# Performance work log

Hardware: AMD Instinct MI355X
Metric: run time of the kernel (lower is better)

The kernel has to match this reference:

```python
import jax, jax.numpy as jnp
import numpy as np

NB_CLS, NB_QRY, NB_SHOT, FEAT_DIM = 5, 75, 5, 640
Q_STEPS, LR_DNI, HID = 3, 1e-3, 4096
N = NB_CLS + NB_QRY           # nodes in similarity graph (80)
M = 1 + N                     # subgraph size (81)
# strict upper triangle of MxM minus the query-query block (matches triu_index_input)
_t = np.ones((M, M)); _t[1 + NB_CLS:, 1 + NB_CLS:] = 0
_t = np.triu(_t, 1)
MASK_IDX = jnp.asarray(np.flatnonzero(_t.ravel() == 1))
DNI_IN = int(MASK_IDX.shape[0])  # 465


def _pairwise(supp, query):
    feat = jnp.concatenate([supp, query], 0)
    nrm = jnp.maximum(jnp.linalg.norm(feat, axis=-1, keepdims=True), 1e-12)
    feat = feat / nrm
    sim = feat @ feat.T                      # (N, N)
    sim_ss = sim[:NB_CLS, :NB_CLS]
    sim_qq = sim[NB_CLS:, NB_CLS:]
    sim_sq = sim[:NB_CLS, NB_CLS:]
    sim_feat_support = jnp.concatenate([sim_ss, sim_sq], 1).T   # (N, nb_cls)
    sim_feat_query = jnp.concatenate([sim_sq, sim_qq], 0)       # (N, nb_qry)
    return sim_feat_support, sim_feat_query, sim_sq


def _subgraph(sim_s, sim_q):
    # topk indices are constants wrt grad (no_grad in torch; ints in jax)
    idx_q = jax.lax.top_k(sim_q, NB_QRY)[1] + NB_CLS
    idx_s = jax.lax.top_k(sim_s, NB_CLS)[1]
    index = jnp.concatenate([jnp.arange(N, dtype=idx_s.dtype)[:, None], idx_s, idx_q], 1)  # (N, M)
    sim = jnp.concatenate([sim_s, sim_q], 1)                     # (N, N)
    sub = sim[index[:, :, None], index[:, None, :]]              # (N, M, M) batched gather
    return sub.reshape(N, M * M)[:, MASK_IDX]                    # (N, DNI_IN)


def _dni(x, W1, b1, W2, b2, W3, b3):
    h = jax.nn.relu(x @ W1.T + b1)
    h = jax.nn.relu(h @ W2.T + b2)
    return h @ W3.T + b3


def _refine(supp, query, ds, dq):
    for _ in range(Q_STEPS):
        inputs, vjp = jax.vjp(lambda s: _subgraph(*_pairwise(s, query)[:2]), supp)
        supp = supp - LR_DNI * vjp(_dni(inputs, *ds))[0]
        inputs, vjp = jax.vjp(lambda q: _subgraph(*_pairwise(supp, q)[:2]), query)
        query = query - LR_DNI * vjp(_dni(inputs, *dq))[0]
    return supp, query


def setup_inputs() -> dict:
    key = jax.random.key(0)
    ks = jax.random.split(key, 16)
    d = {
        "feat_support": jax.random.normal(ks[0], (NB_CLS, NB_SHOT, FEAT_DIM), jnp.float32),
        "feat_query": jax.random.normal(ks[1], (NB_QRY, FEAT_DIM), jnp.float32),
        "scale_cls": jnp.full((1,), 10.0, jnp.float32),
    }
    names = ["ds_W1", "ds_b1", "ds_W2", "ds_b2", "ds_W3", "ds_b3",
             "dq_W1", "dq_b1", "dq_W2", "dq_b2", "dq_W3", "dq_b3"]
    shapes = [(HID, DNI_IN), (HID,), (HID, HID), (HID,), (DNI_IN, HID), (DNI_IN,)] * 2
    for i, (n, sh) in enumerate(zip(names, shapes)):
        d[n] = jax.random.normal(ks[2 + i], sh, jnp.float32) * 0.02
    return d


def reference(feat_support, feat_query, scale_cls,
              ds_W1, ds_b1, ds_W2, ds_b2, ds_W3, ds_b3,
              dq_W1, dq_b1, dq_W2, dq_b2, dq_W3, dq_b3):
    supp = feat_support.mean(1)                                  # (nb_cls, feat_dim)
    ds = (ds_W1, ds_b1, ds_W2, ds_b2, ds_W3, ds_b3)
    dq = (dq_W1, dq_b1, dq_W2, dq_b2, dq_W3, dq_b3)
    supp, query = _refine(supp, feat_query, ds, dq)
    _, _, sim_sq = _pairwise(supp, query)
    return (sim_sq * scale_cls).T                                # (nb_qry, nb_cls)
```

## Files before the change

### kernel.cpp

```cpp
#include <hip/hip_runtime.h>

#define NCLS 5
#define NQRY 75
#define NTOT 80
#define FD   640
#define HIDN 4096
#define DNIN 465
#define KPAD 512
#define NPAD 512
#define LRDNI 1e-3f

#define KS1 4
#define KS2 16
#define KS3 32

typedef short  v8s __attribute__((ext_vector_type(8)));
typedef float  v4f __attribute__((ext_vector_type(4)));

__device__ __forceinline__ ushort f2bf(float x) {
    uint u = __float_as_uint(x);
    u = (u + 0x7FFFu + ((u >> 16) & 1u)) >> 16;
    return (ushort)u;
}
__device__ __forceinline__ uint pk2(float a, float b) {
    return (uint)f2bf(a) | ((uint)f2bf(b) << 16);
}

__global__ void k_setup(const float* __restrict__ fs, const float* __restrict__ fq,
                        const float* __restrict__ W1s, const float* __restrict__ W1q,
                        const float* __restrict__ W2s, const float* __restrict__ W2q,
                        const float* __restrict__ W3s, const float* __restrict__ W3q,
                        ushort* __restrict__ W1bs, ushort* __restrict__ W1bq,
                        ushort* __restrict__ W2bs, ushort* __restrict__ W2bq,
                        ushort* __restrict__ W3bs, ushort* __restrict__ W3bq,
                        float* __restrict__ supp, float* __restrict__ qbuf) {
    int stride = gridDim.x * 256;
    int tid = blockIdx.x * 256 + threadIdx.x;
    for (int o = tid; o < 524288; o += stride) {
        int oo = o & 262143;
        const float* Ws = (o < 262144) ? W1s : W1q;
        ushort* Wd = (o < 262144) ? W1bs : W1bq;
        int l = oo & 63, ks = (oo >> 6) & 15, nt = oo >> 10;
        int n = nt * 16 + (l & 15), kb = ks * 32 + ((l >> 4) << 3);
        ushort tmp[8];
        #pragma unroll
        for (int j = 0; j < 8; j++) {
            int k = kb + j;
            tmp[j] = (k < DNIN) ? f2bf(Ws[n * DNIN + k]) : (ushort)0;
        }
        *(uint4*)(Wd + (size_t)oo * 8) = *(uint4*)tmp;
    }
    for (int o = tid; o < 524288; o += stride) {
        int oo = o & 262143;
        const float* Ws = (o < 262144) ? W3s : W3q;
        ushort* Wd = (o < 262144) ? W3bs : W3bq;
        int l = oo & 63, ks = (oo >> 6) & 127, nt = oo >> 13;
        int n = nt * 16 + (l & 15), kb = ks * 32 + ((l >> 4) << 3);
        uint4 q;
        if (n < DNIN) {
            float4 f0 = *(const float4*)(Ws + (size_t)n * HIDN + kb);
            float4 f1 = *(const float4*)(Ws + (size_t)n * HIDN + kb + 4);
            q.x = pk2(f0.x, f0.y); q.y = pk2(f0.z, f0.w);
            q.z = pk2(f1.x, f1.y); q.w = pk2(f1.z, f1.w);
        } else q = (uint4){0, 0, 0, 0};
        *(uint4*)(Wd + (size_t)oo * 8) = q;
    }
    for (int o = tid; o < 4194304; o += stride) {
        int oo = o & 2097151;
        const float* Ws = (o < 2097152) ? W2s : W2q;
        ushort* Wd = (o < 2097152) ? W2bs : W2bq;
        int l = oo & 63, ks = (oo >> 6) & 127, nt = oo >> 13;
        int n = nt * 16 + (l & 15), kb = ks * 32 + ((l >> 4) << 3);
        float4 f0 = *(const float4*)(Ws + (size_t)n * HIDN + kb);
        float4 f1 = *(const float4*)(Ws + (size_t)n * HIDN + kb + 4);
        uint4 q;
        q.x = pk2(f0.x, f0.y); q.y = pk2(f0.z, f0.w);
        q.z = pk2(f1.x, f1.y); q.w = pk2(f1.z, f1.w);
        *(uint4*)(Wd + (size_t)oo * 8) = q;
    }
    for (int o = tid; o < NCLS * FD; o += stride) {
        int c = o / FD, d = o % FD;
        float s = 0.f;
        #pragma unroll
        for (int t = 0; t < 5; t++) s += fs[(c * 5 + t) * FD + d];
        supp[o] = s * 0.2f;
    }
    for (int o = tid; o < NQRY * FD / 4; o += stride)
        ((float4*)qbuf)[o] = ((const float4*)fq)[o];
}

__device__ __forceinline__ const float* rowptr(const float* supp, const float* qbuf, int r) {
    return (r < NCLS) ? (supp + r * FD) : (qbuf + (r - NCLS) * FD);
}

template<bool FIN>
__global__ void k_simrank(const float* __restrict__ supp, const float* __restrict__ qbuf,
                          float* __restrict__ f, float* __restrict__ nrm,
                          float* __restrict__ S, int* __restrict__ perm,
                          const float* __restrict__ scale, float* __restrict__ out) {
    __shared__ float fi[FD];
    __shared__ float row[NTOT];
    __shared__ float ssh[NTOT];
    int i = blockIdx.x;
    int t = threadIdx.x;
    const float* ri = rowptr(supp, qbuf, i);
    for (int u = t; u < FD; u += 128) fi[u] = ri[u];
    __syncthreads();
    float dot = 0.f;
    if (t < NTOT) {
        const float* rj = rowptr(supp, qbuf, t);
        float ss = 0.f;
        for (int k = 0; k < FD; k += 4) {
            float4 a = *(const float4*)(fi + k);
            float4 b = *(const float4*)(rj + k);
            dot += a.x * b.x + a.y * b.y + a.z * b.z + a.w * b.w;
            ss  += b.x * b.x + b.y * b.y + b.z * b.z + b.w * b.w;
        }
        ssh[t] = ss;
    }
    __syncthreads();
    float ni = fmaxf(sqrtf(ssh[i]), 1e-12f);
    float inv_i = 1.0f / ni;
    if (t < NTOT) {
        float nt = fmaxf(sqrtf(ssh[t]), 1e-12f);
        float val = dot * inv_i / nt;
        if (FIN) {
            if (t >= NCLS) out[(t - NCLS) * NCLS + i] = val * scale[0];
        } else {
            row[t] = val;
            S[i * NTOT + t] = val;
        }
    }
    if (FIN) return;
    __syncthreads();
    for (int u = t; u < FD; u += 128) f[i * FD + u] = fi[u] * inv_i;
    if (t == 0) { nrm[i] = ni; perm[i * 81] = i; }
    if (t < NCLS) {
        float v = row[t]; int rank = 0;
        for (int k = 0; k < NCLS; k++) {
            float w = row[k];
            if (w > v || (w == v && k < t)) rank++;
        }
        perm[i * 81 + 1 + rank] = t;
    } else if (t < NTOT) {
        int j = t - NCLS; float v = row[t]; int rank = 0;
        for (int k = NCLS; k < NTOT; k++) {
            float w = row[k];
            if (w > v || (w == v && (k - NCLS) < j)) rank++;
        }
        perm[i * 81 + 6 + rank] = t;
    }
}

__device__ __forceinline__ void mask_ab(int m, int& a, int& b) {
    int start = 0, len = 80, aa = 0;
    while (m >= start + len) { start += len; len--; aa++; }
    a = aa; b = aa + 1 + (m - start);
}

__global__ void k_gather(const float* __restrict__ S, const int* __restrict__ perm,
                         ushort* __restrict__ Xb, float* __restrict__ Gs) {
    __shared__ int p[81];
    int i = blockIdx.x;
    int t = threadIdx.x;
    if (t < 81) p[t] = perm[i * 81 + t];
    if (t < NTOT) Gs[i * NTOT + t] = 0.f;
    __syncthreads();
    if (t < DNIN) {
        int a, b; mask_ab(t, a, b);
        Xb[i * KPAD + t] = f2bf(S[p[a] * NTOT + p[b]]);
    } else if (t < KPAD) {
        Xb[i * KPAD + t] = 0;
    }
}

template<int NT, int KSTEPS>
__global__ __launch_bounds__(256) void k_gemm(
        const ushort* __restrict__ A, int lda,
        const ushort* __restrict__ Bf, int nks,
        float* __restrict__ C, int ldc) {
    int tid = threadIdx.x;
    int w = tid >> 6, lane = tid & 63, l16 = lane & 15, quad = lane >> 4;
    int n0 = blockIdx.x * (NT * 64) + w * NT * 16;
    int kc0 = blockIdx.y * (KSTEPS * 32);
    const ushort* Ap = A + l16 * lda + kc0 + quad * 8;
    const ushort* Bp = Bf + ((size_t)(n0 >> 4) * nks + (kc0 >> 5)) * 512 + lane * 8;

    v4f acc[5][NT];
    #pragma unroll
    for (int mt = 0; mt < 5; mt++)
        #pragma unroll
        for (int nt = 0; nt < NT; nt++) acc[mt][nt] = (v4f){0.f, 0.f, 0.f, 0.f};

    #pragma unroll
    for (int s = 0; s < KSTEPS; s++) {
        v8s a[5], b[NT];
        #pragma unroll
        for (int mt = 0; mt < 5; mt++)
            a[mt] = *(const v8s*)(Ap + mt * 16 * lda + s * 32);
        #pragma unroll
        for (int nt = 0; nt < NT; nt++)
            b[nt] = *(const v8s*)(Bp + ((size_t)nt * nks + s) * 512);
        #pragma unroll
        for (int mt = 0; mt < 5; mt++)
            #pragma unroll
            for (int nt = 0; nt < NT; nt++)
                acc[mt][nt] = __builtin_amdgcn_mfma_f32_16x16x32_bf16(a[mt], b[nt], acc[mt][nt], 0, 0, 0);
    }
    float* Cp = C + (size_t)blockIdx.y * 80 * ldc;
    #pragma unroll
    for (int nt = 0; nt < NT; nt++) {
        int col = n0 + nt * 16 + l16;
        #pragma unroll
        for (int mt = 0; mt < 5; mt++)
            #pragma unroll
            for (int r = 0; r < 4; r++)
                Cp[(mt * 16 + quad * 4 + r) * ldc + col] = acc[mt][nt][r];
    }
}

template<int NS>
__global__ void k_ep(const float* __restrict__ P, const float* __restrict__ bias,
                     ushort* __restrict__ H) {
    int idx = blockIdx.x * 256 + threadIdx.x;
    float4 s = ((const float4*)bias)[idx & 1023];
    #pragma unroll
    for (int ks = 0; ks < NS; ks++) {
        float4 p = ((const float4*)P)[ks * (80 * HIDN / 4) + idx];
        s.x += p.x; s.y += p.y; s.z += p.z; s.w += p.w;
    }
    uint2 q;
    q.x = pk2(fmaxf(s.x, 0.f), fmaxf(s.y, 0.f));
    q.y = pk2(fmaxf(s.z, 0.f), fmaxf(s.w, 0.f));
    ((uint2*)H)[idx] = q;
}

__global__ void k_scatter(const float* __restrict__ P3, const float* __restrict__ b3,
                          const int* __restrict__ perm, float* __restrict__ Gs) {
    __shared__ int p[81];
    int i = blockIdx.x;
    int t = threadIdx.x;
    if (t < 81) p[t] = perm[i * 81 + t];
    __syncthreads();
    if (t < DNIN) {
        float g = b3[t];
        #pragma unroll
        for (int ks = 0; ks < KS3; ks++) g += P3[ks * (80 * NPAD) + i * NPAD + t];
        int a, b; mask_ab(t, a, b);
        atomicAdd(&Gs[p[a] * NTOT + p[b]], g);
    }
}

__global__ void k_bwd(const float* __restrict__ Gs, const float* __restrict__ f,
                      const float* __restrict__ nrm, float* __restrict__ target,
                      int row0) {
    int r = row0 + blockIdx.x;
    __shared__ float cj[NTOT];
    __shared__ float red[2];
    int t = threadIdx.x;
    if (t < NTOT) cj[t] = Gs[r * NTOT + t] + Gs[t * NTOT + r];
    __syncthreads();
    float df[5] = {0.f, 0.f, 0.f, 0.f, 0.f};
    for (int j = 0; j < NTOT; j++) {
        float c = cj[j];
        const float* fj = f + j * FD;
        #pragma unroll
        for (int u = 0; u < 5; u++) df[u] += c * fj[t + 128 * u];
    }
    const float* fr = f + r * FD;
    float frv[5]; float partial = 0.f;
    #pragma unroll
    for (int u = 0; u < 5; u++) { frv[u] = fr[t + 128 * u]; partial += df[u] * frv[u]; }
    #pragma unroll
    for (int o = 32; o > 0; o >>= 1) partial += __shfl_xor(partial, o, 64);
    if ((t & 63) == 0) red[t >> 6] = partial;
    __syncthreads();
    float dot = red[0] + red[1];
    float invn = 1.0f / nrm[r];
    float* dst = target + blockIdx.x * FD;
    #pragma unroll
    for (int u = 0; u < 5; u++) {
        float dx = (df[u] - dot * frv[u]) * invn;
        dst[t + 128 * u] -= LRDNI * dx;
    }
}

extern "C" void kernel_launch(void* const* d_in, const int* in_sizes, int n_in,
                              void* d_out, int out_size, void* d_ws, size_t ws_size,
                              hipStream_t stream) {
    const float* fs    = (const float*)d_in[0];
    const float* fq    = (const float*)d_in[1];
    const float* scale = (const float*)d_in[2];
    const float* W[12];
    for (int i = 0; i < 12; i++) W[i] = (const float*)d_in[3 + i];

    float* base = (float*)d_ws;
    float* supp = base;
    float* qbuf = supp + 3200;
    float* f    = qbuf + 48000;
    float* nrm  = f + 51200;
    float* S    = nrm + 96;
    int*   perm = (int*)(S + 6400);
    float* P1   = (float*)(perm + 6496);
    float* P2   = P1 + (size_t)KS1 * 80 * HIDN;
    float* P3   = P2 + (size_t)KS2 * 80 * HIDN;
    float* Gs   = P3 + (size_t)KS3 * 80 * NPAD;
    ushort* Xb  = (ushort*)(Gs + 6400);
    ushort* H1b = Xb + 80 * KPAD;
    ushort* H2b = H1b + 80 * HIDN;
    ushort* W1b_ds = H2b + 80 * HIDN;
    ushort* W1b_dq = W1b_ds + HIDN * KPAD;
    ushort* W3b_ds = W1b_dq + HIDN * KPAD;
    ushort* W3b_dq = W3b_ds + NPAD * HIDN;
    ushort* W2b_ds = W3b_dq + NPAD * HIDN;
    ushort* W2b_dq = W2b_ds + (size_t)HIDN * HIDN;

    k_setup<<<1024, 256, 0, stream>>>(fs, fq, W[0], W[6], W[2], W[8], W[4], W[10],
                                      W1b_ds, W1b_dq, W2b_ds, W2b_dq, W3b_ds, W3b_dq,
                                      supp, qbuf);

    for (int step = 0; step < 3; step++) {
        for (int half = 0; half < 2; half++) {
            const float* const* w = (half == 0) ? W : (W + 6);
            const ushort* W1b = (half == 0) ? W1b_ds : W1b_dq;
            const ushort* W2b = (half == 0) ? W2b_ds : W2b_dq;
            const ushort* W3b = (half == 0) ? W3b_ds : W3b_dq;
            k_simrank<false><<<80, 128, 0, stream>>>(supp, qbuf, f, nrm, S, perm, nullptr, nullptr);
            k_gather<<<80, 512, 0, stream>>>(S, perm, Xb, Gs);
            k_gemm<1, 4><<<dim3(64, KS1), 256, 0, stream>>>(Xb, KPAD, W1b, 16, P1, HIDN);
            k_ep<KS1><<<320, 256, 0, stream>>>(P1, w[1], H1b);
            k_gemm<2, 8><<<dim3(32, KS2), 256, 0, stream>>>(H1b, HIDN, W2b, 128, P2, HIDN);
            k_ep<KS2><<<320, 256, 0, stream>>>(P2, w[3], H2b);
            k_gemm<1, 4><<<dim3(8, KS3), 256, 0, stream>>>(H2b, HIDN, W3b, 128, P3, NPAD);
            k_scatter<<<80, 512, 0, stream>>>(P3, w[5], perm, Gs);
            if (half == 0) k_bwd<<<5, 128, 0, stream>>>(Gs, f, nrm, supp, 0);
            else           k_bwd<<<75, 128, 0, stream>>>(Gs, f, nrm, qbuf, NCLS);
        }
    }
    k_simrank<true><<<5, 128, 0, stream>>>(supp, qbuf, f, nrm, S, perm, scale, (float*)d_out);
}
```

Measured before the change: 631.1 us.

## Retile layer-2 GEMM split-K and flatten setup conversion to one pass per thread

The hidden-layer GEMM now uses fewer split-K slices (16 to 8) with a different tile shape (1x16 instead of 2x8, 64 column blocks). This cuts partial-sum traffic and the reduction work in the epilogue. The setup kernel drops its grid-stride loops: each thread converts a fixed set of W2 elements for both networks, plus one W1, one W3 and one small copy element, launched on a 2048-block grid. This gives more loads in flight per thread, but it depends on the grid exactly covering the element counts.

```diff
diff --git a/kernel.cpp b/kernel.cpp
--- a/kernel.cpp
+++ b/kernel.cpp
@@ -11,7 +11,7 @@
 #define LRDNI 1e-3f
 
 #define KS1 4
-#define KS2 16
+#define KS2 8
 #define KS3 32
 
 typedef short  v8s __attribute__((ext_vector_type(8)));
@@ -26,7 +26,8 @@
     return (uint)f2bf(a) | ((uint)f2bf(b) << 16);
 }
 
-__global__ void k_setup(const float* __restrict__ fs, const float* __restrict__ fq,
+__global__ __launch_bounds__(256) void k_setup(
+                        const float* __restrict__ fs, const float* __restrict__ fq,
                         const float* __restrict__ W1s, const float* __restrict__ W1q,
                         const float* __restrict__ W2s, const float* __restrict__ W2q,
                         const float* __restrict__ W3s, const float* __restrict__ W3q,
@@ -34,12 +35,31 @@
                         ushort* __restrict__ W2bs, ushort* __restrict__ W2bq,
                         ushort* __restrict__ W3bs, ushort* __restrict__ W3bq,
                         float* __restrict__ supp, float* __restrict__ qbuf) {
-    int stride = gridDim.x * 256;
     int tid = blockIdx.x * 256 + threadIdx.x;
-    for (int o = tid; o < 524288; o += stride) {
-        int oo = o & 262143;
-        const float* Ws = (o < 262144) ? W1s : W1q;
-        ushort* Wd = (o < 262144) ? W1bs : W1bq;
+
+    #pragma unroll
+    for (int i = 0; i < 4; i++) {
+        int oo = tid + i * 524288;
+        int l = oo & 63, ks = (oo >> 6) & 127, nt = oo >> 13;
+        int n = nt * 16 + (l & 15), kb = ks * 32 + ((l >> 4) << 3);
+        size_t src = (size_t)n * HIDN + kb;
+        float4 s0 = *(const float4*)(W2s + src);
+        float4 s1 = *(const float4*)(W2s + src + 4);
+        float4 t0 = *(const float4*)(W2q + src);
+        float4 t1 = *(const float4*)(W2q + src + 4);
+        uint4 qa, qb;
+        qa.x = pk2(s0.x, s0.y); qa.y = pk2(s0.z, s0.w);
+        qa.z = pk2(s1.x, s1.y); qa.w = pk2(s1.z, s1.w);
+        qb.x = pk2(t0.x, t0.y); qb.y = pk2(t0.z, t0.w);
+        qb.z = pk2(t1.x, t1.y); qb.w = pk2(t1.z, t1.w);
+        *(uint4*)(W2bs + (size_t)oo * 8) = qa;
+        *(uint4*)(W2bq + (size_t)oo * 8) = qb;
+    }
+
+    {
+        int oo = tid & 262143;
+        const float* Ws = (tid < 262144) ? W1s : W1q;
+        ushort* Wd = (tid < 262144) ? W1bs : W1bq;
         int l = oo & 63, ks = (oo >> 6) & 15, nt = oo >> 10;
         int n = nt * 16 + (l & 15), kb = ks * 32 + ((l >> 4) << 3);
         ushort tmp[8];
@@ -50,10 +70,11 @@
         }
         *(uint4*)(Wd + (size_t)oo * 8) = *(uint4*)tmp;
     }
-    for (int o = tid; o < 524288; o += stride) {
-        int oo = o & 262143;
-        const float* Ws = (o < 262144) ? W3s : W3q;
-        ushort* Wd = (o < 262144) ? W3bs : W3bq;
+
+    {
+        int oo = tid & 262143;
+        const float* Ws = (tid < 262144) ? W3s : W3q;
+        ushort* Wd = (tid < 262144) ? W3bs : W3bq;
         int l = oo & 63, ks = (oo >> 6) & 127, nt = oo >> 13;
         int n = nt * 16 + (l & 15), kb = ks * 32 + ((l >> 4) << 3);
         uint4 q;
@@ -65,28 +86,16 @@
         } else q = (uint4){0, 0, 0, 0};
         *(uint4*)(Wd + (size_t)oo * 8) = q;
     }
-    for (int o = tid; o < 4194304; o += stride) {
-        int oo = o & 2097151;
-        const float* Ws = (o < 2097152) ? W2s : W2q;
-        ushort* Wd = (o < 2097152) ? W2bs : W2bq;
-        int l = oo & 63, ks = (oo >> 6) & 127, nt = oo >> 13;
-        int n = nt * 16 + (l & 15), kb = ks * 32 + ((l >> 4) << 3);
-        float4 f0 = *(const float4*)(Ws + (size_t)n * HIDN + kb);
-        float4 f1 = *(const float4*)(Ws + (size_t)n * HIDN + kb + 4);
-        uint4 q;
-        q.x = pk2(f0.x, f0.y); q.y = pk2(f0.z, f0.w);
-        q.z = pk2(f1.x, f1.y); q.w = pk2(f1.z, f1.w);
-        *(uint4*)(Wd + (size_t)oo * 8) = q;
-    }
-    for (int o = tid; o < NCLS * FD; o += stride) {
-        int c = o / FD, d = o % FD;
+
+    if (tid < NCLS * FD) {
+        int c = tid / FD, d = tid % FD;
         float s = 0.f;
         #pragma unroll
         for (int t = 0; t < 5; t++) s += fs[(c * 5 + t) * FD + d];
-        supp[o] = s * 0.2f;
-    }
-    for (int o = tid; o < NQRY * FD / 4; o += stride)
-        ((float4*)qbuf)[o] = ((const float4*)fq)[o];
+        supp[tid] = s * 0.2f;
+    }
+    if (tid < NQRY * FD / 4)
+        ((float4*)qbuf)[tid] = ((const float4*)fq)[tid];
 }
 
 __device__ __forceinline__ const float* rowptr(const float* supp, const float* qbuf, int r) {
@@ -315,7 +324,7 @@
     ushort* W2b_ds = W3b_dq + NPAD * HIDN;
     ushort* W2b_dq = W2b_ds + (size_t)HIDN * HIDN;
 
-    k_setup<<<1024, 256, 0, stream>>>(fs, fq, W[0], W[6], W[2], W[8], W[4], W[10],
+    k_setup<<<2048, 256, 0, stream>>>(fs, fq, W[0], W[6], W[2], W[8], W[4], W[10],
                                       W1b_ds, W1b_dq, W2b_ds, W2b_dq, W3b_ds, W3b_dq,
                                       supp, qbuf);
 
@@ -329,7 +338,7 @@
             k_gather<<<80, 512, 0, stream>>>(S, perm, Xb, Gs);
             k_gemm<1, 4><<<dim3(64, KS1), 256, 0, stream>>>(Xb, KPAD, W1b, 16, P1, HIDN);
             k_ep<KS1><<<320, 256, 0, stream>>>(P1, w[1], H1b);
-            k_gemm<2, 8><<<dim3(32, KS2), 256, 0, stream>>>(H1b, HIDN, W2b, 128, P2, HIDN);
+            k_gemm<1, 16><<<dim3(64, KS2), 256, 0, stream>>>(H1b, HIDN, W2b, 128, P2, HIDN);
             k_ep<KS2><<<320, 256, 0, stream>>>(P2, w[3], H2b);
             k_gemm<1, 4><<<dim3(8, KS3), 256, 0, stream>>>(H2b, HIDN, W3b, 128, P3, NPAD);
             k_scatter<<<80, 512, 0, stream>>>(P3, w[5], perm, Gs);
```

After: 656.9 us. +4.1%, slower.
